# Optimization experiments

Measured on AMD Instinct MI355X. Metric: run time of the kernel, lower is better.

## Reference

```python
import jax, jax.numpy as jnp
import numpy as np

B, S, T, F, C = 32, 8, 1024, 128, 1
CLIP = 10.0

def setup_inputs() -> dict:
    key = jax.random.key(0)
    k1, k2 = jax.random.split(key)
    specs = jax.random.normal(k1, (B, S, T, F, C), dtype=jnp.float32)
    mask = jax.random.randint(k2, (B, S), 0, 2, dtype=jnp.int32)
    return {"specs": specs, "mask": mask}

def _axis_mask(key, dim, max_w, dtype):
    # Vectorized equivalent of one time/freq mask applied with prob 0.65 per (b,s) sample.
    k1, k2, k3 = jax.random.split(key, 3)
    width = jax.random.randint(k1, (B, S), 1, max_w + 1)              # [B,S]
    u = jax.random.uniform(k2, (B, S))
    start = jnp.floor(u * jnp.maximum(1, dim - width)).astype(jnp.int32)
    idx = jnp.arange(dim)                                             # [dim]
    zeroed = (idx[None, None, :] >= start[:, :, None]) & (idx[None, None, :] < (start + width)[:, :, None])
    apply = jax.random.uniform(k3, (B, S)) > 0.35
    m = jnp.where(apply[:, :, None], ~zeroed, True)                   # [B,S,dim] bool
    return m.astype(dtype)

def reference(specs, mask):
    # training=True, enabled=True path
    key = jax.random.key(42)
    kt1, kt2, kf1, kf2, kn_a, kn, ks_a, ks = jax.random.split(key, 8)
    dt = specs.dtype
    max_t = max(1, int(T * 0.12))
    max_f = max(1, int(F * 0.12))

    tm = _axis_mask(kt1, T, max_t, dt) * _axis_mask(kt2, T, max_t, dt)   # [B,S,T]
    fm = _axis_mask(kf1, F, max_f, dt) * _axis_mask(kf2, F, max_f, dt)   # [B,S,F]

    s = specs * tm[:, :, :, None, None] * fm[:, :, None, :, None]

    # additive noise with prob 0.55
    apply_n = (jax.random.uniform(kn_a, (B, S)) > 0.45).astype(dt)
    noise = 0.06 * jax.random.normal(kn, specs.shape, dtype=dt)
    s = s + noise * apply_n[:, :, None, None, None]

    # random scale with prob 0.5
    sc = jax.random.uniform(ks, (B, S), minval=0.85, maxval=1.15, dtype=dt)
    apply_s = jax.random.uniform(ks_a, (B, S)) > 0.5
    sc = jnp.where(apply_s, sc, jnp.ones_like(sc))
    s = s * sc[:, :, None, None, None]

    s = jnp.clip(s, -CLIP, CLIP)

    sensor_on = mask.astype(jnp.float32) > 0.5                           # [B,S]
    return jnp.where(sensor_on[:, :, None, None, None], s, specs)
```

## Files before the change

kernel.cpp:

```cpp
#include <hip/hip_runtime.h>
#include <stdint.h>

namespace {

constexpr int kB = 32, kS = 8, kT = 1024, kF = 128;
constexpr int kBS = kB * kS;
constexpr int kSlice = kT * kF;
constexpr uint32_t kSpanT = 122;
constexpr uint32_t kSpanF = 15;

typedef float f32x4 __attribute__((ext_vector_type(4)));

struct BSParams {
  int ts1, te1, ts2, te2;
  int fs1, fe1, fs2, fe2;
  float scale;
  int apply_n;
  uint32_t kn0, kn1;
};

__device__ __forceinline__ uint32_t rotl32(uint32_t v, int d) {
  return (v << d) | (v >> (32 - d));
}

__device__ __forceinline__ void tf2x32(uint32_t k0, uint32_t k1, uint32_t x0, uint32_t x1,
                                       uint32_t& o0, uint32_t& o1) {
  const uint32_t ks0 = k0, ks1 = k1, ks2 = k0 ^ k1 ^ 0x1BD11BDAu;
  x0 += ks0; x1 += ks1;
  x0 += x1; x1 = rotl32(x1, 13); x1 ^= x0;
  x0 += x1; x1 = rotl32(x1, 15); x1 ^= x0;
  x0 += x1; x1 = rotl32(x1, 26); x1 ^= x0;
  x0 += x1; x1 = rotl32(x1, 6);  x1 ^= x0;
  x0 += ks1; x1 += ks2 + 1u;
  x0 += x1; x1 = rotl32(x1, 17); x1 ^= x0;
  x0 += x1; x1 = rotl32(x1, 29); x1 ^= x0;
  x0 += x1; x1 = rotl32(x1, 16); x1 ^= x0;
  x0 += x1; x1 = rotl32(x1, 24); x1 ^= x0;
  x0 += ks2; x1 += ks0 + 2u;
  x0 += x1; x1 = rotl32(x1, 13); x1 ^= x0;
  x0 += x1; x1 = rotl32(x1, 15); x1 ^= x0;
  x0 += x1; x1 = rotl32(x1, 26); x1 ^= x0;
  x0 += x1; x1 = rotl32(x1, 6);  x1 ^= x0;
  x0 += ks0; x1 += ks1 + 3u;
  x0 += x1; x1 = rotl32(x1, 17); x1 ^= x0;
  x0 += x1; x1 = rotl32(x1, 29); x1 ^= x0;
  x0 += x1; x1 = rotl32(x1, 16); x1 ^= x0;
  x0 += x1; x1 = rotl32(x1, 24); x1 ^= x0;
  x0 += ks1; x1 += ks2 + 4u;
  x0 += x1; x1 = rotl32(x1, 13); x1 ^= x0;
  x0 += x1; x1 = rotl32(x1, 15); x1 ^= x0;
  x0 += x1; x1 = rotl32(x1, 26); x1 ^= x0;
  x0 += x1; x1 = rotl32(x1, 6);  x1 ^= x0;
  x0 += ks2; x1 += ks0 + 5u;
  o0 = x0; o1 = x1;
}

__device__ __forceinline__ uint32_t bits32(uint32_t k0, uint32_t k1, uint32_t ctr) {
  uint32_t o0, o1;
  tf2x32(k0, k1, 0u, ctr, o0, o1);
  return o0 ^ o1;
}

__device__ __forceinline__ float u01(uint32_t bits) {
  return __uint_as_float(0x3f800000u | (bits >> 9)) - 1.0f;
}

__device__ __forceinline__ float erfinv_fast(float x) {
  float t = fmaf(-x, x, 1.0f);
  float w = -0.69314718f * __builtin_amdgcn_logf(t);
  float wm = w - 2.5f;
  float p = 2.81022636e-08f;
  p = fmaf(p, wm, 3.43273939e-07f);
  p = fmaf(p, wm, -3.5233877e-06f);
  p = fmaf(p, wm, -4.39150654e-06f);
  p = fmaf(p, wm, 0.00021858087f);
  p = fmaf(p, wm, -0.00125372503f);
  p = fmaf(p, wm, -0.00417768164f);
  p = fmaf(p, wm, 0.246640727f);
  p = fmaf(p, wm, 1.50140941f);
  float tail = fmaf(1.0003f, __builtin_amdgcn_sqrtf(w), -0.1623f);
  p = (w < 5.0f) ? p : tail;
  return p * x;
}

__device__ void axis_params(uint32_t K0, uint32_t K1, int dim, uint32_t span, uint32_t i,
                            int& start_out, int& end_out) {
  uint32_t k10, k11, k20, k21, k30, k31, a0, a1, b0, b1;
  tf2x32(K0, K1, 0u, 0u, k10, k11);
  tf2x32(K0, K1, 0u, 1u, k20, k21);
  tf2x32(K0, K1, 0u, 2u, k30, k31);
  tf2x32(k10, k11, 0u, 0u, a0, a1);
  tf2x32(k10, k11, 0u, 1u, b0, b1);
  uint32_t hi = bits32(a0, a1, i);
  uint32_t lo = bits32(b0, b1, i);
  uint32_t mult = 65536u % span;
  mult = (mult * mult) % span;
  uint32_t off = ((hi % span) * mult + (lo % span)) % span;
  int width = 1 + (int)off;
  float u = u01(bits32(k20, k21, i));
  int M = dim - width; if (M < 1) M = 1;
  int start = (int)floorf(u * (float)M);
  bool apply = u01(bits32(k30, k31, i)) > 0.35f;
  start_out = start;
  end_out = apply ? (start + width) : start;
}

__device__ BSParams compute_params(uint32_t i) {
  BSParams p;
  uint32_t w0, w1;
  tf2x32(0u, 42u, 0u, 0u, w0, w1); axis_params(w0, w1, kT, kSpanT, i, p.ts1, p.te1);
  tf2x32(0u, 42u, 0u, 1u, w0, w1); axis_params(w0, w1, kT, kSpanT, i, p.ts2, p.te2);
  tf2x32(0u, 42u, 0u, 2u, w0, w1); axis_params(w0, w1, kF, kSpanF, i, p.fs1, p.fe1);
  tf2x32(0u, 42u, 0u, 3u, w0, w1); axis_params(w0, w1, kF, kSpanF, i, p.fs2, p.fe2);
  tf2x32(0u, 42u, 0u, 4u, w0, w1);
  p.apply_n = (u01(bits32(w0, w1, i)) > 0.45f) ? 1 : 0;
  tf2x32(0u, 42u, 0u, 5u, p.kn0, p.kn1);
  tf2x32(0u, 42u, 0u, 6u, w0, w1);
  bool apply_s = u01(bits32(w0, w1, i)) > 0.5f;
  tf2x32(0u, 42u, 0u, 7u, w0, w1);
  float su = u01(bits32(w0, w1, i));
  float sc = fmaxf(0.85f, fmaf(su, 1.15f - 0.85f, 0.85f));
  p.scale = apply_s ? sc : 1.0f;
  return p;
}

__global__ void spec_params_kernel(BSParams* __restrict__ P) {
  uint32_t i = threadIdx.x;
  P[i] = compute_params(i);
}

template <bool USE_WS>
__global__ __launch_bounds__(256) void spec_main_kernel(const float* __restrict__ specs,
                                                        const int* __restrict__ mask,
                                                        float* __restrict__ out,
                                                        const BSParams* __restrict__ P) {
  const int bs = blockIdx.y;
  const int block_off = blockIdx.x * 4096;
  const int tid4 = threadIdx.x * 4;
  const long slice_base = (long)bs * kSlice;

  f32x4 a[4];
  long base[4];
#pragma unroll
  for (int k = 0; k < 4; ++k) {
    base[k] = slice_base + block_off + k * 1024 + tid4;
    a[k] = *reinterpret_cast<const f32x4*>(specs + base[k]);
  }

  if (mask[bs] == 0) {
#pragma unroll
    for (int k = 0; k < 4; ++k)
      __builtin_nontemporal_store(a[k], reinterpret_cast<f32x4*>(out + base[k]));
    return;
  }

  BSParams p;
  if (USE_WS) p = P[bs]; else p = compute_params((uint32_t)bs);

  const float LO = __int_as_float(0xBF7FFFFF);
  const float sc = p.scale;
  const bool noise = (p.apply_n != 0);

#pragma unroll
  for (int k = 0; k < 4; ++k) {
    const int off = block_off + k * 1024 + tid4;
    const int t = off >> 7;
    const int f0 = off & 127;
    const bool tm = !((t >= p.ts1) & (t < p.te1)) && !((t >= p.ts2) & (t < p.te2));
    int lo1 = min(4, max(0, p.fs1 - f0)), hi1 = min(4, max(0, p.fe1 - f0));
    int lo2 = min(4, max(0, p.fs2 - f0)), hi2 = min(4, max(0, p.fe2 - f0));
    uint32_t z1 = ((1u << hi1) - 1u) & ~((1u << lo1) - 1u);
    uint32_t z2 = ((1u << hi2) - 1u) & ~((1u << lo2) - 1u);
    const uint32_t keep = tm ? (0xFu & ~(z1 | z2)) : 0u;

    float v[4] = {a[k].x, a[k].y, a[k].z, a[k].w};
    if (noise) {
      const uint32_t c0 = (uint32_t)base[k];
#pragma unroll
      for (int j = 0; j < 4; ++j) {
        float s = (keep & (1u << j)) ? v[j] : 0.0f;
        const uint32_t bits = bits32(p.kn0, p.kn1, c0 + (uint32_t)j);
        float u1 = __uint_as_float(0x3f800000u | (bits >> 9));
        float x = fmaxf(LO, fmaf(u1, 2.0f, -2.0f) + LO);
        s = fmaf(0.08485281374f, erfinv_fast(x), s);
        s *= sc;
        v[j] = fminf(10.0f, fmaxf(-10.0f, s));
      }
    } else {
#pragma unroll
      for (int j = 0; j < 4; ++j) {
        float s = (keep & (1u << j)) ? v[j] : 0.0f;
        s *= sc;
        v[j] = fminf(10.0f, fmaxf(-10.0f, s));
      }
    }
    f32x4 r = {v[0], v[1], v[2], v[3]};
    __builtin_nontemporal_store(r, reinterpret_cast<f32x4*>(out + base[k]));
  }
}

}

extern "C" void kernel_launch(void* const* d_in, const int* in_sizes, int n_in,
                              void* d_out, int out_size, void* d_ws, size_t ws_size,
                              hipStream_t stream) {
  const float* specs = (const float*)d_in[0];
  const int* mask = (const int*)d_in[1];
  float* out = (float*)d_out;

  dim3 grid(kSlice / 4096, kBS);
  dim3 block(256);

  if (ws_size >= sizeof(BSParams) * kBS) {
    BSParams* P = (BSParams*)d_ws;
    hipLaunchKernelGGL(spec_params_kernel, dim3(1), dim3(kBS), 0, stream, P);
    hipLaunchKernelGGL((spec_main_kernel<true>), grid, block, 0, stream, specs, mask, out, P);
  } else {
    hipLaunchKernelGGL((spec_main_kernel<false>), grid, block, 0, stream, specs, mask, out,
                       (const BSParams*)nullptr);
  }
}
```

Baseline: 54.77 us.

## Parallelize params kernel across 1024 threads and double per-block work

```diff
diff --git a/kernel.cpp b/kernel.cpp
--- a/kernel.cpp
+++ b/kernel.cpp
@@ -124,9 +124,41 @@
   return p;
 }
 
-__global__ void spec_params_kernel(BSParams* __restrict__ P) {
-  uint32_t i = threadIdx.x;
-  P[i] = compute_params(i);
+__global__ __launch_bounds__(1024) void spec_params_kernel(BSParams* __restrict__ P) {
+  __shared__ BSParams sp[kBS];
+  __shared__ float ssc[kBS];
+  __shared__ int ssa[kBS];
+  const uint32_t bs = threadIdx.x & 255u;
+  const uint32_t unit = threadIdx.x >> 8;
+  uint32_t w0, w1;
+  tf2x32(0u, 42u, 0u, unit, w0, w1);
+  int s, e;
+  if (unit < 2) axis_params(w0, w1, kT, kSpanT, bs, s, e);
+  else          axis_params(w0, w1, kF, kSpanF, bs, s, e);
+  if (unit == 0) { sp[bs].ts1 = s; sp[bs].te1 = e; }
+  else if (unit == 1) { sp[bs].ts2 = s; sp[bs].te2 = e; }
+  else if (unit == 2) { sp[bs].fs1 = s; sp[bs].fe1 = e; }
+  else { sp[bs].fs2 = s; sp[bs].fe2 = e; }
+  if (unit == 0) {
+    tf2x32(0u, 42u, 0u, 4u, w0, w1);
+    sp[bs].apply_n = (u01(bits32(w0, w1, bs)) > 0.45f) ? 1 : 0;
+  } else if (unit == 1) {
+    uint32_t n0, n1;
+    tf2x32(0u, 42u, 0u, 5u, n0, n1);
+    sp[bs].kn0 = n0; sp[bs].kn1 = n1;
+  } else if (unit == 2) {
+    tf2x32(0u, 42u, 0u, 6u, w0, w1);
+    ssa[bs] = (u01(bits32(w0, w1, bs)) > 0.5f) ? 1 : 0;
+  } else {
+    tf2x32(0u, 42u, 0u, 7u, w0, w1);
+    float su = u01(bits32(w0, w1, bs));
+    ssc[bs] = fmaxf(0.85f, fmaf(su, 1.15f - 0.85f, 0.85f));
+  }
+  __syncthreads();
+  if (unit == 0) {
+    sp[bs].scale = ssa[bs] ? ssc[bs] : 1.0f;
+    P[bs] = sp[bs];
+  }
 }
 
 template <bool USE_WS>
@@ -134,48 +166,49 @@
                                                         const int* __restrict__ mask,
                                                         float* __restrict__ out,
                                                         const BSParams* __restrict__ P) {
-  const int bs = blockIdx.y;
-  const int block_off = blockIdx.x * 4096;
+  const int blk = blockIdx.x;
+  const int bs = blk & 255;
+  const int block_off = (blk >> 8) * 8192;
   const int tid4 = threadIdx.x * 4;
   const long slice_base = (long)bs * kSlice;
-
-  f32x4 a[4];
-  long base[4];
-#pragma unroll
-  for (int k = 0; k < 4; ++k) {
-    base[k] = slice_base + block_off + k * 1024 + tid4;
-    a[k] = *reinterpret_cast<const f32x4*>(specs + base[k]);
-  }
+  const long base0 = slice_base + block_off + tid4;
+
+  f32x4 a[8];
+#pragma unroll
+  for (int k = 0; k < 8; ++k)
+    a[k] = *reinterpret_cast<const f32x4*>(specs + base0 + k * 1024);
 
   if (mask[bs] == 0) {
 #pragma unroll
-    for (int k = 0; k < 4; ++k)
-      __builtin_nontemporal_store(a[k], reinterpret_cast<f32x4*>(out + base[k]));
+    for (int k = 0; k < 8; ++k)
+      __builtin_nontemporal_store(a[k], reinterpret_cast<f32x4*>(out + base0 + k * 1024));
     return;
   }
 
   BSParams p;
   if (USE_WS) p = P[bs]; else p = compute_params((uint32_t)bs);
 
+  const int f0 = tid4 & 127;
+  int lo1 = min(4, max(0, p.fs1 - f0)), hi1 = min(4, max(0, p.fe1 - f0));
+  int lo2 = min(4, max(0, p.fs2 - f0)), hi2 = min(4, max(0, p.fe2 - f0));
+  uint32_t z1 = ((1u << hi1) - 1u) & ~((1u << lo1) - 1u);
+  uint32_t z2 = ((1u << hi2) - 1u) & ~((1u << lo2) - 1u);
+  const uint32_t fkeep = 0xFu & ~(z1 | z2);
+
+  const int t0 = (block_off + tid4) >> 7;
   const float LO = __int_as_float(0xBF7FFFFF);
   const float sc = p.scale;
   const bool noise = (p.apply_n != 0);
 
 #pragma unroll
-  for (int k = 0; k < 4; ++k) {
-    const int off = block_off + k * 1024 + tid4;
-    const int t = off >> 7;
-    const int f0 = off & 127;
+  for (int k = 0; k < 8; ++k) {
+    const int t = t0 + k * 8;
     const bool tm = !((t >= p.ts1) & (t < p.te1)) && !((t >= p.ts2) & (t < p.te2));
-    int lo1 = min(4, max(0, p.fs1 - f0)), hi1 = min(4, max(0, p.fe1 - f0));
-    int lo2 = min(4, max(0, p.fs2 - f0)), hi2 = min(4, max(0, p.fe2 - f0));
-    uint32_t z1 = ((1u << hi1) - 1u) & ~((1u << lo1) - 1u);
-    uint32_t z2 = ((1u << hi2) - 1u) & ~((1u << lo2) - 1u);
-    const uint32_t keep = tm ? (0xFu & ~(z1 | z2)) : 0u;
+    const uint32_t keep = tm ? fkeep : 0u;
 
     float v[4] = {a[k].x, a[k].y, a[k].z, a[k].w};
     if (noise) {
-      const uint32_t c0 = (uint32_t)base[k];
+      const uint32_t c0 = (uint32_t)(base0 + k * 1024);
 #pragma unroll
       for (int j = 0; j < 4; ++j) {
         float s = (keep & (1u << j)) ? v[j] : 0.0f;
@@ -195,7 +228,7 @@
       }
     }
     f32x4 r = {v[0], v[1], v[2], v[3]};
-    __builtin_nontemporal_store(r, reinterpret_cast<f32x4*>(out + base[k]));
+    __builtin_nontemporal_store(r, reinterpret_cast<f32x4*>(out + base0 + k * 1024));
   }
 }
 
@@ -208,12 +241,12 @@
   const int* mask = (const int*)d_in[1];
   float* out = (float*)d_out;
 
-  dim3 grid(kSlice / 4096, kBS);
+  dim3 grid(kBS * (kSlice / 8192));
   dim3 block(256);
 
   if (ws_size >= sizeof(BSParams) * kBS) {
     BSParams* P = (BSParams*)d_ws;
-    hipLaunchKernelGGL(spec_params_kernel, dim3(1), dim3(kBS), 0, stream, P);
+    hipLaunchKernelGGL(spec_params_kernel, dim3(1), dim3(1024), 0, stream, P);
     hipLaunchKernelGGL((spec_main_kernel<true>), grid, block, 0, stream, specs, mask, out, P);
   } else {
     hipLaunchKernelGGL((spec_main_kernel<false>), grid, block, 0, stream, specs, mask, out,
```

Result: slower. 72.09 us (+31.6%).
